# Performance work log

Hardware: AMD Instinct MI355X
Metric: run time of the kernel (lower is better)

## Reference

```python
import jax, jax.numpy as jnp
import numpy as np

LEVELS = (1, 2, 4)
NHEAD = 4
LN_EPS = 1e-5


def _layernorm(x, g, b):
    m = jnp.mean(x, axis=-1, keepdims=True)
    v = jnp.mean((x - m) ** 2, axis=-1, keepdims=True)
    return (x - m) * jax.lax.rsqrt(v + LN_EPS) * g + b


def _spp_pool(x, starts, ends):
    # Exact AdaptiveAvgPool1d over per-proposal segments via inclusive-prefix-sum.
    # x: [B,C,T]; starts/ends: [B,P] int. Returns [B, P, C*sum(LEVELS)].
    B, C, T = x.shape
    P = starts.shape[1]
    xt = jnp.transpose(x, (0, 2, 1))  # [B,T,C]
    csum = jnp.concatenate([jnp.zeros((B, 1, C), x.dtype), jnp.cumsum(xt, axis=1)], axis=1)  # [B,T+1,C]
    n = ends - starts  # [B,P], always >= 1
    feats = []
    for L in LEVELS:
        i = jnp.arange(L)
        lo = (starts[..., None] + (i * n[..., None]) // L).reshape(B, P * L)
        hi = (starts[..., None] + ((i + 1) * n[..., None] + L - 1) // L).reshape(B, P * L)
        slo = jnp.take_along_axis(csum, lo[..., None], axis=1)  # [B,P*L,C]
        shi = jnp.take_along_axis(csum, hi[..., None], axis=1)
        mean = (shi - slo) / (hi - lo).astype(x.dtype)[..., None]
        # torch view(N, C*L) flattens [C,L] C-major -> transpose bins to last axis
        feats.append(mean.reshape(B, P, L, C).transpose(0, 1, 3, 2).reshape(B, P, C * L))
    return jnp.concatenate(feats, axis=-1)


def _encoder_layer(x, qkv_w, qkv_b, out_w, out_b, g1, b1, w1, bb1, w2, bb2, g2, b2):
    # Post-norm nn.TransformerEncoderLayer with exact-erf gelu, dropout=0 (eval)
    B, P, d = x.shape
    dh = d // NHEAD
    qkv = x @ qkv_w.T + qkv_b  # [B,P,3d]
    q, k, v = jnp.split(qkv, 3, axis=-1)
    sh = lambda t: t.reshape(B, P, NHEAD, dh).transpose(0, 2, 1, 3)  # [B,H,P,dh]
    q, k, v = sh(q), sh(k), sh(v)
    scale = 1.0 / float(np.sqrt(dh))
    attn = jax.nn.softmax(jnp.einsum('bhqd,bhkd->bhqk', q, k) * scale, axis=-1)
    o = jnp.einsum('bhqk,bhkd->bhqd', attn, v).transpose(0, 2, 1, 3).reshape(B, P, d)
    o = o @ out_w.T + out_b
    x = _layernorm(x + o, g1, b1)
    h = jax.nn.gelu(x @ w1.T + bb1, approximate=False) @ w2.T + bb2
    return _layernorm(x + h, g2, b2)


def _forward(x, proposal_boxes, proj_w, proj_b, pos_w1, pos_b1, pos_w2, pos_b2,
             qkv_w, qkv_b, out_w, out_b, ln1_g, ln1_b, ff1_w, ff1_b,
             ff2_w, ff2_b, ln2_g, ln2_b, cls_w, cls_b, det_w, det_b):
    B, C, T = x.shape
    P = proposal_boxes.shape[1]
    starts = jnp.clip(proposal_boxes[..., 0], 0, T - 1)
    ends = jnp.clip(proposal_boxes[..., 1], 1, T)
    ends = jnp.where(ends <= starts, jnp.minimum(starts + 1, T), ends)
    feats = _spp_pool(x, starts, ends)  # [B,P,spp_out_dim]
    s_f = proposal_boxes[..., 0].astype(x.dtype)
    e_f = proposal_boxes[..., 1].astype(x.dtype)
    centers = (s_f + e_f) / 2.0
    lengths = jnp.maximum(e_f - s_f, 1.0)
    pos_feat = jnp.stack([centers / T, lengths / T], axis=-1)  # [B,P,2]
    sort_idx = jnp.argsort(centers, axis=1)
    feats_s = jnp.take_along_axis(feats, sort_idx[..., None], axis=1)
    pos_emb = jax.nn.relu(pos_feat @ pos_w1.T + pos_b1) @ pos_w2.T + pos_b2
    pos_emb_s = jnp.take_along_axis(pos_emb, sort_idx[..., None], axis=1)
    tok = feats_s @ proj_w.T + proj_b + pos_emb_s  # [B,P,d]
    for l in range(qkv_w.shape[0]):
        tok = _encoder_layer(tok, qkv_w[l], qkv_b[l], out_w[l], out_b[l],
                             ln1_g[l], ln1_b[l], ff1_w[l], ff1_b[l],
                             ff2_w[l], ff2_b[l], ln2_g[l], ln2_b[l])
    inv = jnp.argsort(sort_idx, axis=1)
    ctx = jnp.take_along_axis(tok, inv[..., None], axis=1)  # [B,P,d]
    class_logits = ctx @ cls_w.T + cls_b  # [B,P,nc]
    det_logits = ctx @ det_w.T + det_b
    class_prob = jax.nn.softmax(class_logits, axis=2)
    det_prob = jax.nn.softmax(det_logits, axis=1)
    joint_prob = class_prob * det_prob
    video_prob = joint_prob.sum(axis=1)
    return video_prob, joint_prob, class_logits, det_logits, ctx


def setup_inputs() -> dict:
    key = jax.random.key(0)
    ks = jax.random.split(key, 32)
    B, C, T, P = 8, 512, 2048, 512
    d, dff, nc, nl = 512, 1024, 30, 2
    spp_out = C * sum(LEVELS)
    s = 0.02
    f32 = jnp.float32
    inp = {
        'x': jax.random.normal(ks[0], (B, C, T), f32),
        'proposal_boxes': jax.random.randint(ks[1], (B, P, 2), 0, T).astype(jnp.int32),
        'proj_w': jax.random.normal(ks[2], (d, spp_out), f32) * s,
        'proj_b': jnp.zeros((d,), f32),
        'pos_w1': jax.random.normal(ks[3], (d, 2), f32) * s,
        'pos_b1': jnp.zeros((d,), f32),
        'pos_w2': jax.random.normal(ks[4], (d, d), f32) * s,
        'pos_b2': jnp.zeros((d,), f32),
        'qkv_w': jax.random.normal(ks[5], (nl, 3 * d, d), f32) * s,
        'qkv_b': jnp.zeros((nl, 3 * d), f32),
        'out_w': jax.random.normal(ks[6], (nl, d, d), f32) * s,
        'out_b': jnp.zeros((nl, d), f32),
        'ln1_g': jnp.ones((nl, d), f32),
        'ln1_b': jnp.zeros((nl, d), f32),
        'ff1_w': jax.random.normal(ks[7], (nl, dff, d), f32) * s,
        'ff1_b': jnp.zeros((nl, dff), f32),
        'ff2_w': jax.random.normal(ks[8], (nl, d, dff), f32) * s,
        'ff2_b': jnp.zeros((nl, d), f32),
        'ln2_g': jnp.ones((nl, d), f32),
        'ln2_b': jnp.zeros((nl, d), f32),
        'cls_w': jax.random.normal(ks[9], (nc, d), f32) * s,
        'cls_b': jnp.zeros((nc,), f32),
        'det_w': jax.random.normal(ks[10], (nc, d), f32) * s,
        'det_b': jnp.zeros((nc,), f32),
    }
    return inp


def reference(x, proposal_boxes, proj_w, proj_b, pos_w1, pos_b1, pos_w2, pos_b2,
              qkv_w, qkv_b, out_w, out_b, ln1_g, ln1_b, ff1_w, ff1_b,
              ff2_w, ff2_b, ln2_g, ln2_b, cls_w, cls_b, det_w, det_b):
    return _forward(x, proposal_boxes, proj_w, proj_b, pos_w1, pos_b1, pos_w2, pos_b2,
                    qkv_w, qkv_b, out_w, out_b, ln1_g, ln1_b, ff1_w, ff1_b,
                    ff2_w, ff2_b, ln2_g, ln2_b, cls_w, cls_b, det_w, det_b)
```

## Files before the change

kernel.cpp:

```cpp
#include <hip/hip_runtime.h>

#define TDIM 2048
#define CDIM 512
#define BDIM 8
#define PDIM 512
#define DMODEL 512
#define NCOUT 30
#define SPPOUT 3584
#define AKDIM 4096

typedef __attribute__((ext_vector_type(8))) short short8;
typedef __attribute__((ext_vector_type(4))) short short4v;
typedef __attribute__((ext_vector_type(4))) float f32x4;

typedef const __attribute__((address_space(1))) void* as1cv;
typedef __attribute__((address_space(3))) void* as3v;

__device__ __forceinline__ void gl_lds16(const short* g, short* l){
  __builtin_amdgcn_global_load_lds((as1cv)g, (as3v)l, 16, 0, 0);
}

__device__ __forceinline__ short f2b(float f){
  unsigned u = __float_as_uint(f);
  unsigned r = (u + 0x7fffu + ((u >> 16) & 1u)) >> 16;
  return (short)r;
}

__device__ __forceinline__ float waveSum(float v){
#pragma unroll
  for (int o = 32; o > 0; o >>= 1) v += __shfl_xor(v, o);
  return v;
}
__device__ __forceinline__ float waveMax(float v){
#pragma unroll
  for (int o = 32; o > 0; o >>= 1) v = fmaxf(v, __shfl_xor(v, o));
  return v;
}

__global__ __launch_bounds__(512) void k0(
    const float* __restrict__ x, const int* __restrict__ boxes,
    const float* __restrict__ pw, const float* __restrict__ pw2,
    const float* __restrict__ qw, const float* __restrict__ ow,
    const float* __restrict__ f1, const float* __restrict__ f2,
    const float* __restrict__ cl, const float* __restrict__ dt,
    const float* __restrict__ pb, const float* __restrict__ pb2,
    const float* __restrict__ cb, const float* __restrict__ db,
    float* __restrict__ W, float* __restrict__ tot,
    int* __restrict__ sidx, float* __restrict__ out,
    short* __restrict__ Wc, short* __restrict__ Wd,
    float* __restrict__ bc, float* __restrict__ bh)
{
  __shared__ unsigned key[PDIM];
  int blk = blockIdx.x, t = threadIdx.x;
  if (blk < 128){
    int b = blk >> 4, ch = blk & 15;
    int c = t;
    const float* xp = x + ((size_t)(b * CDIM + c)) * TDIM + ch * 128;
    float* wp = W + ((size_t)b * TDIM + ch * 128) * CDIM + c;
    float run = 0.f;
    for (int tl = 0; tl < 128; tl += 4){
      float4 v = *(const float4*)(xp + tl);
      run += v.x; wp[(size_t)(tl + 0) * CDIM] = run;
      run += v.y; wp[(size_t)(tl + 1) * CDIM] = run;
      run += v.z; wp[(size_t)(tl + 2) * CDIM] = run;
      run += v.w; wp[(size_t)(tl + 3) * CDIM] = run;
    }
    tot[((size_t)b * 16 + ch) * CDIM + c] = run;
  } else if (blk < 136){
    int b = blk - 128;
    if (b == 0 && t < 240) out[t] = 0.f;
    int s = boxes[(size_t)(b * PDIM + t) * 2];
    int e = boxes[(size_t)(b * PDIM + t) * 2 + 1];
    key[t] = ((unsigned)(s + e) << 9) | (unsigned)t;
    __syncthreads();
    for (int k = 2; k <= PDIM; k <<= 1){
      for (int j = k >> 1; j > 0; j >>= 1){
        int ixj = t ^ j;
        if (ixj > t){
          unsigned a = key[t], c2 = key[ixj];
          bool up = ((t & k) == 0);
          bool doswap = up ? (a > c2) : (a < c2);
          if (doswap){ key[t] = c2; key[ixj] = a; }
        }
        __syncthreads();
      }
    }
    sidx[b * PDIM + t] = (int)(key[t] & 511u);
  } else {
    int i = (blk - 136) * 512 + t;
    if (i < 2097152){
      int r = i >> 12, k = i & 4095;
      float v = (k < SPPOUT) ? pw[(size_t)r * SPPOUT + k] : pw2[(size_t)r * DMODEL + (k - SPPOUT)];
      Wc[i] = f2b(v);
    } else if (i < 6322176){
      int j = i - 2097152;
      float v;
      if (j < 1572864) v = qw[j];
      else if (j < 2097152) v = ow[j - 1572864];
      else if (j < 3145728) v = f1[j - 2097152];
      else if (j < 4194304) v = f2[j - 3145728];
      else if (j < 4209664) v = cl[j - 4194304];
      else v = dt[j - 4209664];
      Wd[j] = f2b(v);
    } else {
      int k = i - 6322176;
      if (k < 512) bc[k] = pb[k] + pb2[k];
      else if (k < 572) bh[k - 512] = (k < 542) ? cb[k - 512] : db[k - 542];
    }
  }
}

__global__ void koff(const float* __restrict__ tot, float* __restrict__ off){
  int b = blockIdx.x >> 1, cg = blockIdx.x & 1;
  int c = cg * 256 + threadIdx.x;
  float run = 0.f;
  for (int ch = 0; ch < 16; ++ch){
    off[((size_t)b * 16 + ch) * CDIM + c] = run;
    run += tot[((size_t)b * 16 + ch) * CDIM + c];
  }
}

__global__ void kspp(const float* __restrict__ W, const float* __restrict__ off,
                     const int* __restrict__ boxes, const int* __restrict__ sidx,
                     const float* __restrict__ pw1, const float* __restrict__ pb1,
                     short* __restrict__ A){
  int blk = blockIdx.x;
  int b = blk >> 9, j = blk & 511;
  int p = sidx[b * PDIM + j];
  int s0 = boxes[(size_t)(b * PDIM + p) * 2];
  int e0 = boxes[(size_t)(b * PDIM + p) * 2 + 1];
  int start = min(max(s0, 0), TDIM - 1);
  int end   = min(max(e0, 1), TDIM);
  if (end <= start) end = min(start + 1, TDIM);
  int n = end - start;

  int lo[7], hi[7];
  {
    const int Ls[3] = {1, 2, 4};
    int q = 0;
    for (int li = 0; li < 3; ++li){
      int L = Ls[li];
      for (int i = 0; i < L; ++i){
        lo[q] = start + (i * n) / L;
        hi[q] = start + ((i + 1) * n + L - 1) / L;
        ++q;
      }
    }
  }
  float inv[7];
#pragma unroll
  for (int q = 0; q < 7; ++q) inv[q] = 1.f / (float)(hi[q] - lo[q]);

  int R[10] = { start - 1, end - 1, hi[1] - 1, lo[2] - 1, hi[3] - 1,
                lo[4] - 1, hi[4] - 1, lo[5] - 1, hi[5] - 1, lo[6] - 1 };

  float s_f = (float)s0, e_f = (float)e0;
  float px = (s_f + e_f) * 0.5f / (float)TDIM;
  float py = fmaxf(e_f - s_f, 1.f) / (float)TDIM;
  short* Ar = A + (size_t)(b * PDIM + j) * AKDIM;
  const float* Wb = W + (size_t)b * TDIM * CDIM;
  const float* ob = off + (size_t)b * 16 * CDIM;
#pragma unroll
  for (int cc = 0; cc < 2; ++cc){
    int c = threadIdx.x + cc * 256;
    float F[10];
#pragma unroll
    for (int u = 0; u < 10; ++u){
      int r = R[u];
      F[u] = (r < 0) ? 0.f : (Wb[(size_t)r * CDIM + c] + ob[(r >> 7) * CDIM + c]);
    }
    Ar[c]              = f2b((F[1] - F[0]) * inv[0]);
    Ar[512  + c * 2]   = f2b((F[2] - F[0]) * inv[1]);
    Ar[513  + c * 2]   = f2b((F[1] - F[3]) * inv[2]);
    Ar[1536 + c * 4]   = f2b((F[4] - F[0]) * inv[3]);
    Ar[1537 + c * 4]   = f2b((F[6] - F[5]) * inv[4]);
    Ar[1538 + c * 4]   = f2b((F[8] - F[7]) * inv[5]);
    Ar[1539 + c * 4]   = f2b((F[1] - F[9]) * inv[6]);
    float hv = pw1[c * 2] * px + pw1[c * 2 + 1] * py + pb1[c];
    Ar[SPPOUT + c] = f2b(fmaxf(hv, 0.f));
  }
}

template<int BN, int SWZ = 0>
__global__ __launch_bounds__(256) void gemm_bt(
    int M, int N, int K,
    const short* __restrict__ A, int lda, long long sAb, long long sAh,
    const short* __restrict__ B, int ldb, long long sBb, long long sBh,
    float* __restrict__ Cf, short* __restrict__ Cb, int ldc, long long sCb, long long sCh,
    int hdiv, float alpha,
    const float* __restrict__ bias, const float* __restrict__ resid, int act,
    short* __restrict__ Vtp)
{
  constexpr int JF = BN / 32;
  __shared__ short smem[128 * 64 + BN * 64];
  short* As = smem;
  short* Bs = smem + 128 * 64;
  int bx = blockIdx.x, by = blockIdx.y, bz = blockIdx.z;
  if constexpr (SWZ){
    int nx = gridDim.x, ny = gridDim.y;
    int rt = ny >> 3;
    int flat = (bz * ny + by) * nx + bx;
    int xcd = flat & 7, wl = flat >> 3;
    by = xcd * rt + wl % rt;
    int rest = wl / rt;
    bx = rest % nx;
    bz = rest / nx;
  }
  int zb = bz / hdiv, zh = bz - zb * hdiv;
  A += (size_t)zb * sAb + (size_t)zh * sAh;
  B += (size_t)zb * sBb + (size_t)zh * sBh;
  size_t coff = (size_t)zb * sCb + (size_t)zh * sCh;
  int rowBase = by * 128, colBase = bx * BN;
  int t = threadIdx.x;
  int lane = t & 63;
  int wave = t >> 6;
  int wm = (wave >> 1) * 64, wn = (wave & 1) * (BN / 2);
  int lm = lane & 15, quad = lane >> 4;
  int srow = t >> 3;
  int skw = ((t & 7) * 8) ^ ((srow & 7) * 8);

  const short* Agp[4];
#pragma unroll
  for (int it = 0; it < 4; ++it)
    Agp[it] = A + (size_t)min(rowBase + srow + it * 32, M - 1) * lda + skw;
  const short* Bgp[JF];
#pragma unroll
  for (int it = 0; it < JF; ++it)
    Bgp[it] = B + (size_t)min(colBase + srow + it * 32, N - 1) * ldb + skw;

  f32x4 zero4 = {0.f, 0.f, 0.f, 0.f};
  f32x4 acc[4][JF];
#pragma unroll
  for (int i = 0; i < 4; ++i)
#pragma unroll
    for (int j = 0; j < JF; ++j) acc[i][j] = zero4;

  int axr = (lm & 7) * 8;
  for (int k0 = 0; k0 < K; k0 += 64){
#pragma unroll
    for (int it = 0; it < 4; ++it) gl_lds16(Agp[it] + k0, As + it * 2048 + t * 8);
#pragma unroll
    for (int it = 0; it < JF; ++it) gl_lds16(Bgp[it] + k0, Bs + it * 2048 + t * 8);
    __syncthreads();
#pragma unroll
    for (int h = 0; h < 2; ++h){
      int koff = (h * 32 + quad * 8) ^ axr;
      short8 af[4], bfr[JF];
#pragma unroll
      for (int i = 0; i < 4; ++i)
        af[i] = *(const short8*)(As + (wm + i * 16 + lm) * 64 + koff);
#pragma unroll
      for (int j = 0; j < JF; ++j)
        bfr[j] = *(const short8*)(Bs + (wn + j * 16 + lm) * 64 + koff);
#pragma unroll
      for (int i = 0; i < 4; ++i)
#pragma unroll
        for (int j = 0; j < JF; ++j)
          acc[i][j] = __builtin_amdgcn_mfma_f32_16x16x32_bf16(af[i], bfr[j], acc[i][j], 0, 0, 0);
    }
    __syncthreads();
  }

  if (Vtp && colBase >= 1024){
    short* LT = smem;
#pragma unroll
    for (int i = 0; i < 4; ++i){
#pragma unroll
      for (int j = 0; j < JF; ++j){
        int d = wn + j * 16 + lm;
        int prow = wm + i * 16 + quad * 4;
        short4v pk;
#pragma unroll
        for (int r = 0; r < 4; ++r){
          float v = acc[i][j][r] * alpha;
          if (bias) v += bias[colBase + d];
          pk[r] = f2b(v);
        }
        *(short4v*)(LT + d * 132 + prow) = pk;
      }
    }
    __syncthreads();
    int bb = rowBase >> 9;
    int hh = (colBase - 1024) >> 7;
    int dd0 = (colBase - 1024) & 127;
    int dl = t >> 2, pl = (t & 3) * 32;
    const short* sp = LT + dl * 132 + pl;
    short* dp = Vtp + ((size_t)(bb * 4 + hh)) * 65536 + (size_t)(dd0 + dl) * 512 + (rowBase & 511) + pl;
#pragma unroll
    for (int u = 0; u < 4; ++u) *(short8*)(dp + u * 8) = *(const short8*)(sp + u * 8);
    return;
  }

#pragma unroll
  for (int i = 0; i < 4; ++i){
#pragma unroll
    for (int j = 0; j < JF; ++j){
#pragma unroll
      for (int r = 0; r < 4; ++r){
        int row = rowBase + wm + i * 16 + quad * 4 + r;
        int col = colBase + wn + j * 16 + lm;
        if (row < M && col < N){
          float v = acc[i][j][r] * alpha;
          if (bias) v += bias[col];
          size_t ci = coff + (size_t)row * ldc + col;
          if (resid) v += resid[ci];
          if (act) v = 0.5f * v * (1.f + erff(v * 0.7071067811865476f));
          if (Cf) Cf[ci] = v;
          if (Cb) Cb[ci] = f2b(v);
        }
      }
    }
  }
}

__global__ void kredG1(const float* __restrict__ part, const float* __restrict__ bias,
                       float* __restrict__ tok, short* __restrict__ tokb){
  int idx = blockIdx.x * 256 + threadIdx.x;
  const float4* p = (const float4*)part;
  float4 v0 = p[idx], v1 = p[idx + 524288], v2 = p[idx + 1048576], v3 = p[idx + 1572864];
  float4 bv = ((const float4*)bias)[idx & 127];
  float4 v;
  v.x = v0.x + v1.x + v2.x + v3.x + bv.x;
  v.y = v0.y + v1.y + v2.y + v3.y + bv.y;
  v.z = v0.z + v1.z + v2.z + v3.z + bv.z;
  v.w = v0.w + v1.w + v2.w + v3.w + bv.w;
  ((float4*)tok)[idx] = v;
  short4v s4 = { f2b(v.x), f2b(v.y), f2b(v.z), f2b(v.w) };
  *(short4v*)(tokb + (size_t)idx * 4) = s4;
}

__global__ __launch_bounds__(256) void kflash(const short* __restrict__ qkvb,
                                              const short* __restrict__ Vt,
                                              short* __restrict__ ob){
  __shared__ float Ofs[4][16][128];
  __shared__ float Ml[4][16], Ll[4][16], Fw[4][16], Linv[16];
  int bid = blockIdx.x;
  int bh = bid & 31, qt = bid >> 5;
  int b = bh >> 2, h = bh & 3;
  int t = threadIdx.x;
  int w = t >> 6, lane = t & 63;
  int lm = lane & 15, quad = lane >> 4;
  const float SL2 = 0.1275174468f;

  const short* qbase = qkvb + (size_t)(b * 512 + qt * 16 + lm) * 1536 + h * 128 + quad * 8;
  short8 qf[4];
#pragma unroll
  for (int s = 0; s < 4; ++s) qf[s] = *(const short8*)(qbase + s * 32);

  const short* kbase = qkvb + (size_t)(b * 512) * 1536 + 512 + h * 128 + quad * 8;
  const short* vbase = Vt + (size_t)bh * 65536 + (size_t)lm * 512 + quad * 8;

  f32x4 zero4 = {0.f, 0.f, 0.f, 0.f};
  f32x4 Of[8];
#pragma unroll
  for (int i = 0; i < 8; ++i) Of[i] = zero4;
  float mrun[4] = {-1e30f, -1e30f, -1e30f, -1e30f};
  float lrun[4] = {0.f, 0.f, 0.f, 0.f};
  short* Pw = (short*)&Ofs[w][0][0];

#pragma unroll
  for (int kt = 0; kt < 2; ++kt){
    int kb = w * 128 + kt * 64;
    f32x4 Sf[4];
#pragma unroll
    for (int j = 0; j < 4; ++j) Sf[j] = zero4;
#pragma unroll
    for (int s = 0; s < 4; ++s){
#pragma unroll
      for (int j = 0; j < 4; ++j){
        short8 kf = *(const short8*)(kbase + (size_t)(kb + j * 16 + lm) * 1536 + s * 32);
        Sf[j] = __builtin_amdgcn_mfma_f32_16x16x32_bf16(qf[s], kf, Sf[j], 0, 0, 0);
      }
    }
    float alpha[4];
#pragma unroll
    for (int r = 0; r < 4; ++r){
      float mx = fmaxf(fmaxf(Sf[0][r], Sf[1][r]), fmaxf(Sf[2][r], Sf[3][r])) * SL2;
#pragma unroll
      for (int o = 1; o < 16; o <<= 1) mx = fmaxf(mx, __shfl_xor(mx, o));
      float mnew = fmaxf(mrun[r], mx);
      alpha[r] = exp2f(mrun[r] - mnew);
      float psum = 0.f;
#pragma unroll
      for (int j = 0; j < 4; ++j){
        float p = exp2f(Sf[j][r] * SL2 - mnew);
        Sf[j][r] = p;
        psum += p;
      }
#pragma unroll
      for (int o = 1; o < 16; o <<= 1) psum += __shfl_xor(psum, o);
      lrun[r] = lrun[r] * alpha[r] + psum;
      mrun[r] = mnew;
    }
#pragma unroll
    for (int i = 0; i < 8; ++i)
#pragma unroll
      for (int r = 0; r < 4; ++r) Of[i][r] *= alpha[r];
#pragma unroll
    for (int j = 0; j < 4; ++j)
#pragma unroll
      for (int r = 0; r < 4; ++r){
        int q = quad * 4 + r;
        int key = j * 16 + lm;
        Pw[q * 64 + (key ^ ((q & 7) * 8))] = f2b(Sf[j][r]);
      }
#pragma unroll
    for (int ts = 0; ts < 2; ++ts){
      short8 pa = *(const short8*)(Pw + lm * 64 + (((ts * 32 + quad * 8) ^ ((lm & 7) * 8))));
#pragma unroll
      for (int jd = 0; jd < 8; ++jd){
        short8 vf = *(const short8*)(vbase + (size_t)(jd * 16) * 512 + kb + ts * 32);
        Of[jd] = __builtin_amdgcn_mfma_f32_16x16x32_bf16(pa, vf, Of[jd], 0, 0, 0);
      }
    }
  }

#pragma unroll
  for (int jd = 0; jd < 8; ++jd)
#pragma unroll
    for (int r = 0; r < 4; ++r)
      Ofs[w][quad * 4 + r][jd * 16 + lm] = Of[jd][r];
  if (lm == 0){
#pragma unroll
    for (int r = 0; r < 4; ++r){
      Ml[w][quad * 4 + r] = mrun[r];
      Ll[w][quad * 4 + r] = lrun[r];
    }
  }
  __syncthreads();

  if (t < 64){
    int wv = t >> 4, row = t & 15;
    float M = fmaxf(fmaxf(Ml[0][row], Ml[1][row]), fmaxf(Ml[2][row], Ml[3][row]));
    Fw[wv][row] = exp2f(Ml[wv][row] - M);
    if (wv == 0){
      float lsum = Ll[0][row] * exp2f(Ml[0][row] - M) + Ll[1][row] * exp2f(Ml[1][row] - M)
                 + Ll[2][row] * exp2f(Ml[2][row] - M) + Ll[3][row] * exp2f(Ml[3][row] - M);
      Linv[row] = 1.f / lsum;
    }
  }
  __syncthreads();

  {
    int row = t >> 4, dbase = (t & 15) * 8;
    float f0 = Fw[0][row], f1 = Fw[1][row], f2v = Fw[2][row], f3 = Fw[3][row];
    float li = Linv[row];
    short* dst = ob + ((size_t)(b * 512 + qt * 16 + row)) * 512 + h * 128 + dbase;
#pragma unroll
    for (int u = 0; u < 8; ++u){
      float v = Ofs[0][row][dbase + u] * f0 + Ofs[1][row][dbase + u] * f1
              + Ofs[2][row][dbase + u] * f2v + Ofs[3][row][dbase + u] * f3;
      dst[u] = f2b(v * li);
    }
  }
}

__global__ void klnR(const float* __restrict__ part, const float* __restrict__ bias,
                     const float* __restrict__ resid,
                     const float* __restrict__ g, const float* __restrict__ bb,
                     float* __restrict__ Yf, short* __restrict__ Yb){
  int row = blockIdx.x, lane = threadIdx.x;
  size_t base = (size_t)row * DMODEL;
  float v[8]; float s = 0.f;
#pragma unroll
  for (int i = 0; i < 8; ++i){
    int c = lane + 64 * i;
    v[i] = part[base + c] + part[base + c + 2097152] + bias[c] + resid[base + c];
    s += v[i];
  }
  s = waveSum(s);
  float m = s * (1.f / DMODEL);
  float q = 0.f;
#pragma unroll
  for (int i = 0; i < 8; ++i){ float d = v[i] - m; q += d * d; }
  q = waveSum(q);
  float inv = rsqrtf(q * (1.f / DMODEL) + 1e-5f);
#pragma unroll
  for (int i = 0; i < 8; ++i){
    int c = lane + 64 * i;
    float o = (v[i] - m) * inv * g[c] + bb[c];
    Yf[base + c] = o;
    Yb[base + c] = f2b(o);
  }
}

__global__ void kdetsm(const float* __restrict__ hd, float* __restrict__ dp){
  int b = blockIdx.x / NCOUT, c = blockIdx.x % NCOUT, lane = threadIdx.x;
  float v[8]; float m = -1e30f;
#pragma unroll
  for (int i = 0; i < 8; ++i){
    v[i] = hd[((size_t)(b * PDIM) + lane + 64 * i) * 60 + 30 + c];
    m = fmaxf(m, v[i]);
  }
  m = waveMax(m);
  float s = 0.f;
#pragma unroll
  for (int i = 0; i < 8; ++i){ s += expf(v[i] - m); }
  s = waveSum(s);
  if (lane == 0){
    dp[b * NCOUT + c] = m;
    dp[240 + b * NCOUT + c] = 1.f / s;
  }
}

__global__ void kfinal(const float* __restrict__ hd, const float* __restrict__ dps,
                       const float* __restrict__ tok, const int* __restrict__ sidx,
                       float* __restrict__ out){
  int blk = blockIdx.x;
  int b = blk >> 9, j = blk & 511;
  int lane = threadIdx.x;
  int p = sidx[b * PDIM + j];
  float* video = out;
  float* joint = out + 240;
  float* clso  = out + 123120;
  float* deto  = out + 246000;
  float* ctxo  = out + 368880;
  size_t rs60 = (size_t)(b * PDIM + j) * 60;
  size_t ro = (size_t)(b * PDIM + p) * NCOUT;
  float lc = (lane < NCOUT) ? hd[rs60 + lane] : -1e30f;
  float m = waveMax(lc);
  float e = (lane < NCOUT) ? expf(lc - m) : 0.f;
  float s = waveSum(e);
  float cp = e / s;
  if (lane < NCOUT){
    float dv  = hd[rs60 + 30 + lane];
    float dpv = expf(dv - dps[b * NCOUT + lane]) * dps[240 + b * NCOUT + lane];
    float jp  = cp * dpv;
    clso[ro + lane] = lc;
    deto[ro + lane] = dv;
    joint[ro + lane] = jp;
    atomicAdd(&video[b * NCOUT + lane], jp);
  }
  const float4* tr = (const float4*)(tok + (size_t)(b * PDIM + j) * DMODEL);
  float4* cr = (float4*)(ctxo + (size_t)(b * PDIM + p) * DMODEL);
  for (int c = lane; c < DMODEL / 4; c += 64) cr[c] = tr[c];
}

extern "C" void kernel_launch(void* const* d_in, const int* in_sizes, int n_in,
                              void* d_out, int out_size, void* d_ws, size_t ws_size,
                              hipStream_t stream) {
  const float* x      = (const float*)d_in[0];
  const int*   boxes  = (const int*)d_in[1];
  const float* proj_w = (const float*)d_in[2];
  const float* proj_b = (const float*)d_in[3];
  const float* pos_w1 = (const float*)d_in[4];
  const float* pos_b1 = (const float*)d_in[5];
  const float* pos_w2 = (const float*)d_in[6];
  const float* pos_b2 = (const float*)d_in[7];
  const float* qkv_w  = (const float*)d_in[8];
  const float* qkv_b  = (const float*)d_in[9];
  const float* out_w  = (const float*)d_in[10];
  const float* out_b  = (const float*)d_in[11];
  const float* ln1_g  = (const float*)d_in[12];
  const float* ln1_b  = (const float*)d_in[13];
  const float* ff1_w  = (const float*)d_in[14];
  const float* ff1_b  = (const float*)d_in[15];
  const float* ff2_w  = (const float*)d_in[16];
  const float* ff2_b  = (const float*)d_in[17];
  const float* ln2_g  = (const float*)d_in[18];
  const float* ln2_b  = (const float*)d_in[19];
  const float* cls_w  = (const float*)d_in[20];
  const float* cls_b  = (const float*)d_in[21];
  const float* det_w  = (const float*)d_in[22];
  const float* det_b  = (const float*)d_in[23];
  float* out = (float*)d_out;
  float* ws  = (float*)d_ws;

  const size_t oR1    = 0;
  const size_t oS     = 9437184;
  const size_t oOff   = 17825792;
  const size_t oTok   = 22020096;
  const size_t oTokb  = 24117248;
  const size_t oTok2  = 25165824;
  const size_t oTok2b = 27262976;
  const size_t oWcat  = 28311552;
  const size_t oBcat  = 29360128;
  const size_t oWq    = 29360640;
  const size_t oWo    = 30147072;
  const size_t oWf1   = 30409216;
  const size_t oWf2   = 30933504;
  const size_t oWcls  = 31457792;
  const size_t oTot   = 31473152;
  const size_t oSidx  = 31604224;
  const size_t oBhead = oTot + 65536;

  short* Abf   = (short*)(ws + oR1);
  short* qkvb  = (short*)(ws + oR1);
  short* Vt    = (short*)(ws + oR1 + 3145728);
  short* obufb = (short*)(ws + oR1 + 4194304);
  short* hbufb = (short*)(ws + oR1 + 5242880);
  float* headS = ws + oR1 + 7340032;
  float* dpS   = ws + oR1 + 7585792;
  float* csum  = ws + oS;
  float* Cpart = ws + oS;
  float* Cp2   = ws + oS;
  float* offp  = ws + oOff;
  float* tok   = ws + oTok;
  short* tokb  = (short*)(ws + oTokb);
  float* tok2  = ws + oTok2;
  short* tok2b = (short*)(ws + oTok2b);
  short* Wcatb = (short*)(ws + oWcat);
  float* bcat  = ws + oBcat;
  short* Wq    = (short*)(ws + oWq);
  short* Wo    = (short*)(ws + oWo);
  short* Wf1   = (short*)(ws + oWf1);
  short* Wf2   = (short*)(ws + oWf2);
  short* Whead = (short*)(ws + oWcls);
  float* tot   = ws + oTot;
  int*   sidx  = (int*)(ws + oSidx);
  float* bhead = ws + oBhead;

  k0<<<12486, 512, 0, stream>>>(x, boxes, proj_w, pos_w2, qkv_w, out_w, ff1_w, ff2_w,
                                cls_w, det_w, proj_b, pos_b2, cls_b, det_b,
                                csum, tot, sidx, out, Wcatb, Wq, bcat, bhead);
  koff<<<16, 256, 0, stream>>>(tot, offp);
  kspp<<<BDIM * PDIM, 256, 0, stream>>>(csum, offp, boxes, sidx, pos_w1, pos_b1, Abf);

  gemm_bt<64, 1><<<dim3(8, 32, 4), 256, 0, stream>>>(
      4096, 512, 1024, Abf, 4096, 1024, 0, Wcatb, 4096, 1024, 0,
      Cpart, nullptr, 512, 2097152, 0, 1, 1.f, nullptr, nullptr, 0, nullptr);
  kredG1<<<2048, 256, 0, stream>>>(Cpart, bcat, tok, tokb);

  for (int l = 0; l < 2; ++l){
    const short* qw  = Wq  + (size_t)l * 1536 * 512;
    const short* ow  = Wo  + (size_t)l * 512 * 512;
    const short* f1w = Wf1 + (size_t)l * 1024 * 512;
    const short* f2w = Wf2 + (size_t)l * 512 * 1024;
    const float* qb  = qkv_b + (size_t)l * 1536;
    const float* obv = out_b + (size_t)l * 512;
    const float* f1b = ff1_b + (size_t)l * 1024;
    const float* f2b_ = ff2_b + (size_t)l * 512;

    gemm_bt<64><<<dim3(24, 32, 1), 256, 0, stream>>>(
        4096, 1536, 512, tokb, 512, 0, 0, qw, 512, 0, 0,
        nullptr, qkvb, 1536, 0, 0, 1, 1.f, qb, nullptr, 0, Vt);
    kflash<<<1024, 256, 0, stream>>>(qkvb, Vt, obufb);
    gemm_bt<64><<<dim3(8, 32, 2), 256, 0, stream>>>(
        4096, 512, 256, obufb, 512, 256, 0, ow, 512, 256, 0,
        Cp2, nullptr, 512, 2097152, 0, 1, 1.f, nullptr, nullptr, 0, nullptr);
    klnR<<<4096, 64, 0, stream>>>(Cp2, obv, tok, ln1_g + l * 512, ln1_b + l * 512, tok2, tok2b);
    gemm_bt<64><<<dim3(16, 32, 1), 256, 0, stream>>>(
        4096, 1024, 512, tok2b, 512, 0, 0, f1w, 512, 0, 0,
        nullptr, hbufb, 1024, 0, 0, 1, 1.f, f1b, nullptr, 1, nullptr);
    gemm_bt<64><<<dim3(8, 32, 2), 256, 0, stream>>>(
        4096, 512, 512, hbufb, 1024, 512, 0, f2w, 1024, 512, 0,
        Cp2, nullptr, 512, 2097152, 0, 1, 1.f, nullptr, nullptr, 0, nullptr);
    klnR<<<4096, 64, 0, stream>>>(Cp2, f2b_, tok2, ln2_g + l * 512, ln2_b + l * 512, tok, tokb);
  }

  gemm_bt<64><<<dim3(1, 32, 1), 256, 0, stream>>>(
      4096, 60, 512, tokb, 512, 0, 0, Whead, 512, 0, 0,
      headS, nullptr, 60, 0, 0, 1, 1.f, bhead, nullptr, 0, nullptr);
  kdetsm<<<BDIM * NCOUT, 64, 0, stream>>>(headS, dpS);
  kfinal<<<BDIM * PDIM, 64, 0, stream>>>(headS, dpS, tok, sidx, out);
}
```

Baseline: 490.1 us.

## Fuse classifier head GEMM with detection softmax stats; vectorize SPP gather

Replaces the 32-block head GEMM plus separate detection-softmax kernel with one kernel that uses 480 blocks. Each block computes one head column for one batch with a scalar dot product, and the detection columns also reduce the max and sum-exp in place. This removes a kernel launch and the low-parallelism GEMM tile, at the cost of re-reading the token rows for each of the 60 columns. The SPP pooling writer also now handles two channels per thread using float2 loads and packed short2/4/8 stores instead of scalar ones.

Measured after the change: 502.5 us. +2.5%, slower.

```diff
diff --git a/kernel.cpp b/kernel.cpp
--- a/kernel.cpp
+++ b/kernel.cpp
@@ -11,6 +11,7 @@
 
 typedef __attribute__((ext_vector_type(8))) short short8;
 typedef __attribute__((ext_vector_type(4))) short short4v;
+typedef __attribute__((ext_vector_type(2))) short short2v;
 typedef __attribute__((ext_vector_type(4))) float f32x4;
 
 typedef const __attribute__((address_space(1))) void* as1cv;
@@ -24,6 +25,9 @@
   unsigned u = __float_as_uint(f);
   unsigned r = (u + 0x7fffu + ((u >> 16) & 1u)) >> 16;
   return (short)r;
+}
+__device__ __forceinline__ float b2f(unsigned short u){
+  return __uint_as_float(((unsigned)u) << 16);
 }
 
 __device__ __forceinline__ float waveSum(float v){
@@ -160,25 +164,34 @@
   short* Ar = A + (size_t)(b * PDIM + j) * AKDIM;
   const float* Wb = W + (size_t)b * TDIM * CDIM;
   const float* ob = off + (size_t)b * 16 * CDIM;
-#pragma unroll
-  for (int cc = 0; cc < 2; ++cc){
-    int c = threadIdx.x + cc * 256;
-    float F[10];
-#pragma unroll
-    for (int u = 0; u < 10; ++u){
-      int r = R[u];
-      F[u] = (r < 0) ? 0.f : (Wb[(size_t)r * CDIM + c] + ob[(r >> 7) * CDIM + c]);
-    }
-    Ar[c]              = f2b((F[1] - F[0]) * inv[0]);
-    Ar[512  + c * 2]   = f2b((F[2] - F[0]) * inv[1]);
-    Ar[513  + c * 2]   = f2b((F[1] - F[3]) * inv[2]);
-    Ar[1536 + c * 4]   = f2b((F[4] - F[0]) * inv[3]);
-    Ar[1537 + c * 4]   = f2b((F[6] - F[5]) * inv[4]);
-    Ar[1538 + c * 4]   = f2b((F[8] - F[7]) * inv[5]);
-    Ar[1539 + c * 4]   = f2b((F[1] - F[9]) * inv[6]);
-    float hv = pw1[c * 2] * px + pw1[c * 2 + 1] * py + pb1[c];
-    Ar[SPPOUT + c] = f2b(fmaxf(hv, 0.f));
-  }
+  int c0 = threadIdx.x * 2;
+  float2 F[10];
+#pragma unroll
+  for (int u = 0; u < 10; ++u){
+    int r = R[u];
+    if (r < 0){ F[u].x = 0.f; F[u].y = 0.f; }
+    else {
+      float2 wv = *(const float2*)(Wb + (size_t)r * CDIM + c0);
+      float2 ov = *(const float2*)(ob + (r >> 7) * CDIM + c0);
+      F[u].x = wv.x + ov.x; F[u].y = wv.y + ov.y;
+    }
+  }
+  short2v w1 = { f2b((F[1].x - F[0].x) * inv[0]), f2b((F[1].y - F[0].y) * inv[0]) };
+  *(short2v*)(Ar + c0) = w1;
+  short4v w2 = { f2b((F[2].x - F[0].x) * inv[1]), f2b((F[1].x - F[3].x) * inv[2]),
+                 f2b((F[2].y - F[0].y) * inv[1]), f2b((F[1].y - F[3].y) * inv[2]) };
+  *(short4v*)(Ar + 512 + 2 * c0) = w2;
+  short8 w4 = { f2b((F[4].x - F[0].x) * inv[3]), f2b((F[6].x - F[5].x) * inv[4]),
+                f2b((F[8].x - F[7].x) * inv[5]), f2b((F[1].x - F[9].x) * inv[6]),
+                f2b((F[4].y - F[0].y) * inv[3]), f2b((F[6].y - F[5].y) * inv[4]),
+                f2b((F[8].y - F[7].y) * inv[5]), f2b((F[1].y - F[9].y) * inv[6]) };
+  *(short8*)(Ar + 1536 + 4 * c0) = w4;
+  float4 pwv = *(const float4*)(pw1 + 2 * c0);
+  float2 pbv = *(const float2*)(pb1 + c0);
+  float hv0 = pwv.x * px + pwv.y * py + pbv.x;
+  float hv1 = pwv.z * px + pwv.w * py + pbv.y;
+  short2v wm = { f2b(fmaxf(hv0, 0.f)), f2b(fmaxf(hv1, 0.f)) };
+  *(short2v*)(Ar + SPPOUT + c0) = wm;
 }
 
 template<int BN, int SWZ = 0>
@@ -484,22 +497,53 @@
   }
 }
 
-__global__ void kdetsm(const float* __restrict__ hd, float* __restrict__ dp){
-  int b = blockIdx.x / NCOUT, c = blockIdx.x % NCOUT, lane = threadIdx.x;
-  float v[8]; float m = -1e30f;
-#pragma unroll
-  for (int i = 0; i < 8; ++i){
-    v[i] = hd[((size_t)(b * PDIM) + lane + 64 * i) * 60 + 30 + c];
-    m = fmaxf(m, v[i]);
-  }
-  m = waveMax(m);
-  float s = 0.f;
-#pragma unroll
-  for (int i = 0; i < 8; ++i){ s += expf(v[i] - m); }
-  s = waveSum(s);
-  if (lane == 0){
-    dp[b * NCOUT + c] = m;
-    dp[240 + b * NCOUT + c] = 1.f / s;
+__global__ __launch_bounds__(256) void kheadcol(const short* __restrict__ tokb,
+                                                const short* __restrict__ Whead,
+                                                const float* __restrict__ bhead,
+                                                float* __restrict__ headS,
+                                                float* __restrict__ dp){
+  __shared__ float wf[512];
+  __shared__ float redM[4], redS[4];
+  int b = blockIdx.x / 60, col = blockIdx.x % 60;
+  int t = threadIdx.x;
+  {
+    short2v wv = *(const short2v*)(Whead + col * 512 + t * 2);
+    wf[t * 2]     = b2f((unsigned short)wv[0]);
+    wf[t * 2 + 1] = b2f((unsigned short)wv[1]);
+  }
+  __syncthreads();
+  float bias = bhead[col];
+  float val[2];
+#pragma unroll
+  for (int rr = 0; rr < 2; ++rr){
+    int r = t + rr * 256;
+    const short* row = tokb + ((size_t)(b * 512 + r)) * 512;
+    float acc = 0.f;
+#pragma unroll 8
+    for (int k = 0; k < 512; k += 8){
+      short8 v = *(const short8*)(row + k);
+#pragma unroll
+      for (int u = 0; u < 8; ++u) acc += b2f((unsigned short)v[u]) * wf[k + u];
+    }
+    val[rr] = acc + bias;
+    headS[(size_t)(b * 512 + r) * 60 + col] = val[rr];
+  }
+  if (col >= 30){
+    int lane = t & 63, w = t >> 6;
+    float mx = fmaxf(val[0], val[1]);
+    mx = waveMax(mx);
+    if (lane == 0) redM[w] = mx;
+    __syncthreads();
+    float M = fmaxf(fmaxf(redM[0], redM[1]), fmaxf(redM[2], redM[3]));
+    float se = expf(val[0] - M) + expf(val[1] - M);
+    se = waveSum(se);
+    if (lane == 0) redS[w] = se;
+    __syncthreads();
+    if (t == 0){
+      float S = redS[0] + redS[1] + redS[2] + redS[3];
+      dp[b * NCOUT + (col - 30)] = M;
+      dp[240 + b * NCOUT + (col - 30)] = 1.f / S;
+    }
   }
 }
 
@@ -648,9 +692,6 @@
     klnR<<<4096, 64, 0, stream>>>(Cp2, f2b_, tok2, ln2_g + l * 512, ln2_b + l * 512, tok, tokb);
   }
 
-  gemm_bt<64><<<dim3(1, 32, 1), 256, 0, stream>>>(
-      4096, 60, 512, tokb, 512, 0, 0, Whead, 512, 0, 0,
-      headS, nullptr, 60, 0, 0, 1, 1.f, bhead, nullptr, 0, nullptr);
-  kdetsm<<<BDIM * NCOUT, 64, 0, stream>>>(headS, dpS);
+  kheadcol<<<480, 256, 0, stream>>>(tokb, Whead, bhead, headS, dpS);
   kfinal<<<BDIM * PDIM, 64, 0, stream>>>(headS, dpS, tok, sidx, out);
 }
```
